# Kernel optimization log

Hardware: AMD Instinct MI355X
Metric: run time of the kernel (lower is better)

Reference implementation:

```python
import jax, jax.numpy as jnp
import numpy as np

KERNEL_SIZE = 32
KERNEL_STRIDE = 16
HEAD_NUM_K = 4
HEAD_DIM = 128
BATCH = 4
SEQ_LEN = 16384


def _calc_chunks_with_stride(cu_seqlens_np, chunk_size, stride):
    """Mirror of calc_chunks_with_stride using numpy (index computation on host).

    Returns flat gather indices (num_chunks*chunk_size,) and compressed
    cumulative sequence lengths (batch+1,).
    """
    cu = np.asarray(cu_seqlens_np, dtype=np.int64)
    batch_sizes = cu[1:] - cu[:-1]
    max_seq_len = int(batch_sizes.max())
    max_chunks = max((max_seq_len - chunk_size) // stride + 1, 0)
    offsets = np.arange(0, max_chunks * stride, stride, dtype=np.int64)  # (C,)
    seq_starts = cu[:-1]
    chunk_start = seq_starts[:, None] + offsets[None, :]            # (B, C)
    chunk_end = chunk_start + chunk_size
    valid = chunk_end <= (seq_starts[:, None] + batch_sizes[:, None])  # (B, C)
    valid_starts = chunk_start[valid]                               # (N,)
    inner = np.arange(chunk_size, dtype=np.int64)[None, :]          # (1, K)
    flat_idx = (valid_starts[:, None] + inner).reshape(-1)          # (N*K,)
    n_per_batch = valid.sum(axis=1)
    cu_comp = np.zeros(len(cu), dtype=np.int32)
    cu_comp[1:] = np.cumsum(n_per_batch)
    return flat_idx, cu_comp


def setup_inputs() -> dict:
    key = jax.random.key(0)
    k = jax.random.normal(key, (BATCH * SEQ_LEN, HEAD_NUM_K, HEAD_DIM), dtype=jnp.float32)
    cu_seqlens = jnp.arange(BATCH + 1, dtype=jnp.int32) * SEQ_LEN
    return {"k": k, "cu_seqlens": cu_seqlens}


def reference(k, cu_seqlens):
    # Index computation is data-dependent on concrete cu_seqlens (host-side).
    flat_idx, cu_comp = _calc_chunks_with_stride(np.asarray(cu_seqlens), KERNEL_SIZE, KERNEL_STRIDE)
    idx = jnp.asarray(flat_idx)
    # Gather overlapping chunks: (N*K, H, D) -> (N, K, H, D) -> mean over K.
    gathered = k[idx]
    gathered = gathered.reshape(-1, KERNEL_SIZE, HEAD_NUM_K, HEAD_DIM)
    compressed_k = gathered.mean(axis=1)
    return compressed_k, jnp.asarray(cu_comp)
```

## Files before the change

kernel.cpp:

```cpp
#include <hip/hip_runtime.h>

#define KSIZE   32
#define KSTRIDE 16
#define HK      4
#define HD      128
#define ROW     (HK * HD)
#define ROW4    (ROW / 4)
#define BATCH   4
#define SEQLEN  16384
#define CHUNKS_PER_BATCH ((SEQLEN - KSIZE) / KSTRIDE + 1)
#define TOTAL_CHUNKS     (BATCH * CHUNKS_PER_BATCH)

#define G 3
#define BLOCKS_PER_BATCH (CHUNKS_PER_BATCH / G)
#define TOTAL_BLOCKS     (BATCH * BLOCKS_PER_BATCH)

__global__ __launch_bounds__(128)
void compress_k_fused(const float* __restrict__ k,
                      const int* __restrict__ cu_seqlens,
                      float* __restrict__ out,
                      float* __restrict__ tail) {
    const int blk = blockIdx.x;
    const int b   = blk / BLOCKS_PER_BATCH;
    const int cb  = blk - b * BLOCKS_PER_BATCH;
    const int c0  = cb * G;

    const long start_row = (long)cu_seqlens[b] + (long)c0 * KSTRIDE;
    const float4* __restrict__ src = (const float4*)(k + start_row * ROW);
    const int t = threadIdx.x;

    float4 h[G + 1];
    #pragma unroll
    for (int j = 0; j <= G; ++j) h[j] = make_float4(0.f, 0.f, 0.f, 0.f);

    #pragma unroll
    for (int j = 0; j <= G; ++j) {
        #pragma unroll
        for (int i = 0; i < KSTRIDE; ++i) {
            float4 v = src[(long)(j * KSTRIDE + i) * ROW4 + t];
            h[j].x += v.x; h[j].y += v.y; h[j].z += v.z; h[j].w += v.w;
        }
    }

    const float s = 1.0f / (float)KSIZE;
    const int chunk0 = b * CHUNKS_PER_BATCH + c0;
    #pragma unroll
    for (int g = 0; g < G; ++g) {
        float4 r = make_float4((h[g].x + h[g + 1].x) * s,
                               (h[g].y + h[g + 1].y) * s,
                               (h[g].z + h[g + 1].z) * s,
                               (h[g].w + h[g + 1].w) * s);
        ((float4*)(out + (long)(chunk0 + g) * ROW))[t] = r;
    }

    if (blk == 0 && t == 0) {
        int run = 0;
        tail[0] = 0.0f;
        #pragma unroll
        for (int i = 0; i < BATCH; ++i) {
            const int len = cu_seqlens[i + 1] - cu_seqlens[i];
            const int n = (len >= KSIZE) ? (len - KSIZE) / KSTRIDE + 1 : 0;
            run += n;
            tail[i + 1] = (float)run;
        }
    }
}

extern "C" void kernel_launch(void* const* d_in, const int* in_sizes, int n_in,
                              void* d_out, int out_size, void* d_ws, size_t ws_size,
                              hipStream_t stream) {
    const float* k          = (const float*)d_in[0];
    const int*   cu_seqlens = (const int*)d_in[1];
    float*       out        = (float*)d_out;
    float*       tail       = out + (long)TOTAL_CHUNKS * ROW;

    compress_k_fused<<<TOTAL_BLOCKS, 128, 0, stream>>>(k, cu_seqlens, out, tail);
}
```

Before: 195.0 us.

## Split chunk row sums across four thread groups and remap blocks per XCD

Each block now runs 512 threads. Four groups each sum 4 of the 16 rows per stride segment, and the partial sums are combined through shared memory before the output chunks are written. Block IDs are also remapped so that contiguous chunk ranges land on the same XCD, which is meant to improve L2 reuse of the overlapping rows. The change raises per-block parallelism and memory-level parallelism. In exchange it adds a shared-memory reduction and a barrier, and a quarter of the threads sit idle during the write phase.

New measurement: 199.5 us. +2.3%, slower.

```diff
diff --git a/kernel.cpp b/kernel.cpp
--- a/kernel.cpp
+++ b/kernel.cpp
@@ -14,46 +14,67 @@
 #define G 3
 #define BLOCKS_PER_BATCH (CHUNKS_PER_BATCH / G)
 #define TOTAL_BLOCKS     (BATCH * BLOCKS_PER_BATCH)
+#define NXCD 8
 
-__global__ __launch_bounds__(128)
+__global__ __launch_bounds__(512, 4)
 void compress_k_fused(const float* __restrict__ k,
                       const int* __restrict__ cu_seqlens,
                       float* __restrict__ out,
                       float* __restrict__ tail) {
-    const int blk = blockIdx.x;
+    const int bid = blockIdx.x;
+    const int xcd = bid % NXCD;
+    const int sub = bid / NXCD;
+    const int q8  = TOTAL_BLOCKS / NXCD;
+    const int r8  = TOTAL_BLOCKS % NXCD;
+    const int blk = (xcd < r8 ? xcd * (q8 + 1)
+                              : r8 * (q8 + 1) + (xcd - r8) * q8) + sub;
+
     const int b   = blk / BLOCKS_PER_BATCH;
     const int cb  = blk - b * BLOCKS_PER_BATCH;
     const int c0  = cb * G;
 
     const long start_row = (long)cu_seqlens[b] + (long)c0 * KSTRIDE;
     const float4* __restrict__ src = (const float4*)(k + start_row * ROW);
-    const int t = threadIdx.x;
 
-    float4 h[G + 1];
+    const int t   = threadIdx.x;
+    const int col = t & (ROW4 - 1);
+    const int q   = t >> 7;
+
+    float4 p[G + 1];
     #pragma unroll
-    for (int j = 0; j <= G; ++j) h[j] = make_float4(0.f, 0.f, 0.f, 0.f);
+    for (int j = 0; j <= G; ++j) p[j] = make_float4(0.f, 0.f, 0.f, 0.f);
 
     #pragma unroll
     for (int j = 0; j <= G; ++j) {
         #pragma unroll
-        for (int i = 0; i < KSTRIDE; ++i) {
-            float4 v = src[(long)(j * KSTRIDE + i) * ROW4 + t];
-            h[j].x += v.x; h[j].y += v.y; h[j].z += v.z; h[j].w += v.w;
+        for (int r = 0; r < 4; ++r) {
+            float4 v = src[(long)(j * KSTRIDE + q * 4 + r) * ROW4 + col];
+            p[j].x += v.x; p[j].y += v.y; p[j].z += v.z; p[j].w += v.w;
         }
     }
 
-    const float s = 1.0f / (float)KSIZE;
-    const int chunk0 = b * CHUNKS_PER_BATCH + c0;
+    __shared__ float4 ls[G + 1][4][ROW4];
     #pragma unroll
-    for (int g = 0; g < G; ++g) {
-        float4 r = make_float4((h[g].x + h[g + 1].x) * s,
-                               (h[g].y + h[g + 1].y) * s,
-                               (h[g].z + h[g + 1].z) * s,
-                               (h[g].w + h[g + 1].w) * s);
-        ((float4*)(out + (long)(chunk0 + g) * ROW))[t] = r;
+    for (int j = 0; j <= G; ++j) ls[j][q][col] = p[j];
+    __syncthreads();
+
+    if (q < G) {
+        const int g = q;
+        float4 h = make_float4(0.f, 0.f, 0.f, 0.f);
+        #pragma unroll
+        for (int qq = 0; qq < 4; ++qq) {
+            float4 a = ls[g][qq][col];
+            float4 c = ls[g + 1][qq][col];
+            h.x += a.x + c.x; h.y += a.y + c.y;
+            h.z += a.z + c.z; h.w += a.w + c.w;
+        }
+        const float s = 1.0f / (float)KSIZE;
+        h.x *= s; h.y *= s; h.z *= s; h.w *= s;
+        const int chunk0 = b * CHUNKS_PER_BATCH + c0;
+        ((float4*)(out + (long)(chunk0 + g) * ROW))[col] = h;
     }
 
-    if (blk == 0 && t == 0) {
+    if (bid == 0 && t == 0) {
         int run = 0;
         tail[0] = 0.0f;
         #pragma unroll
@@ -74,5 +95,5 @@
     float*       out        = (float*)d_out;
     float*       tail       = out + (long)TOTAL_CHUNKS * ROW;
 
-    compress_k_fused<<<TOTAL_BLOCKS, 128, 0, stream>>>(k, cu_seqlens, out, tail);
+    compress_k_fused<<<TOTAL_BLOCKS, 512, 0, stream>>>(k, cu_seqlens, out, tail);
 }
```

## Use one block per chunk with XCD-aware block remapping for L2 reuse

Applied to the files above, without the earlier changes.

Each block now produces a single output chunk instead of a group of three. Block IDs are remapped so that consecutive chunks land on the same XCD, which lets the overlapping half-windows be shared through that XCD's L2. The cost is twice the raw global loads per output compared with the grouped version, in exchange for more blocks and less per-thread register state.

New measurement: 201.4 us. 3.2% more time.

```diff
diff --git a/kernel.cpp b/kernel.cpp
--- a/kernel.cpp
+++ b/kernel.cpp
@@ -10,50 +10,46 @@
 #define SEQLEN  16384
 #define CHUNKS_PER_BATCH ((SEQLEN - KSIZE) / KSTRIDE + 1)
 #define TOTAL_CHUNKS     (BATCH * CHUNKS_PER_BATCH)
-
-#define G 3
-#define BLOCKS_PER_BATCH (CHUNKS_PER_BATCH / G)
-#define TOTAL_BLOCKS     (BATCH * BLOCKS_PER_BATCH)
+#define NXCD 8
 
 __global__ __launch_bounds__(128)
 void compress_k_fused(const float* __restrict__ k,
                       const int* __restrict__ cu_seqlens,
                       float* __restrict__ out,
                       float* __restrict__ tail) {
-    const int blk = blockIdx.x;
-    const int b   = blk / BLOCKS_PER_BATCH;
-    const int cb  = blk - b * BLOCKS_PER_BATCH;
-    const int c0  = cb * G;
+    const int bid = blockIdx.x;
+    const int xcd = bid % NXCD;
+    const int sub = bid / NXCD;
+    const int q8  = TOTAL_CHUNKS / NXCD;
+    const int r8  = TOTAL_CHUNKS % NXCD;
+    const int blk = (xcd < r8 ? xcd * (q8 + 1)
+                              : r8 * (q8 + 1) + (xcd - r8) * q8) + sub;
 
-    const long start_row = (long)cu_seqlens[b] + (long)c0 * KSTRIDE;
+    const int b = blk / CHUNKS_PER_BATCH;
+    const int c = blk - b * CHUNKS_PER_BATCH;
+
+    const long start_row = (long)cu_seqlens[b] + (long)c * KSTRIDE;
     const float4* __restrict__ src = (const float4*)(k + start_row * ROW);
     const int t = threadIdx.x;
 
-    float4 h[G + 1];
+    float4 h0 = make_float4(0.f, 0.f, 0.f, 0.f);
+    float4 h1 = make_float4(0.f, 0.f, 0.f, 0.f);
     #pragma unroll
-    for (int j = 0; j <= G; ++j) h[j] = make_float4(0.f, 0.f, 0.f, 0.f);
-
-    #pragma unroll
-    for (int j = 0; j <= G; ++j) {
-        #pragma unroll
-        for (int i = 0; i < KSTRIDE; ++i) {
-            float4 v = src[(long)(j * KSTRIDE + i) * ROW4 + t];
-            h[j].x += v.x; h[j].y += v.y; h[j].z += v.z; h[j].w += v.w;
-        }
+    for (int i = 0; i < KSTRIDE; ++i) {
+        float4 a = src[(long)i * ROW4 + t];
+        float4 c2 = src[(long)(KSTRIDE + i) * ROW4 + t];
+        h0.x += a.x;  h0.y += a.y;  h0.z += a.z;  h0.w += a.w;
+        h1.x += c2.x; h1.y += c2.y; h1.z += c2.z; h1.w += c2.w;
     }
 
     const float s = 1.0f / (float)KSIZE;
-    const int chunk0 = b * CHUNKS_PER_BATCH + c0;
-    #pragma unroll
-    for (int g = 0; g < G; ++g) {
-        float4 r = make_float4((h[g].x + h[g + 1].x) * s,
-                               (h[g].y + h[g + 1].y) * s,
-                               (h[g].z + h[g + 1].z) * s,
-                               (h[g].w + h[g + 1].w) * s);
-        ((float4*)(out + (long)(chunk0 + g) * ROW))[t] = r;
-    }
+    float4 r = make_float4((h0.x + h1.x) * s,
+                           (h0.y + h1.y) * s,
+                           (h0.z + h1.z) * s,
+                           (h0.w + h1.w) * s);
+    ((float4*)(out + (long)blk * ROW))[t] = r;
 
-    if (blk == 0 && t == 0) {
+    if (bid == 0 && t == 0) {
         int run = 0;
         tail[0] = 0.0f;
         #pragma unroll
@@ -74,5 +70,5 @@
     float*       out        = (float*)d_out;
     float*       tail       = out + (long)TOTAL_CHUNKS * ROW;
 
-    compress_k_fused<<<TOTAL_BLOCKS, 128, 0, stream>>>(k, cu_seqlens, out, tail);
+    compress_k_fused<<<TOTAL_CHUNKS, 128, 0, stream>>>(k, cu_seqlens, out, tail);
 }
```
